# Kernel tuning notes

Hardware: AMD Instinct MI355X
Metric: run time of the kernel (lower is better)

The kernel has to match this reference:

```python
import jax, jax.numpy as jnp
import numpy as np

N_NODES = 100000
N_EDGES = 500000
DIM = 128
HID = 128

def setup_inputs() -> dict:
    key = jax.random.key(0)
    k1, k2, k3, k4, k5, k6 = jax.random.split(key, 6)
    z = jax.random.normal(k1, (N_NODES, DIM), dtype=jnp.float32)
    edge_index = jax.random.randint(k2, (2, N_EDGES), 0, N_NODES, dtype=jnp.int64)
    # Linear params (torch default init: U(-1/sqrt(fan_in), 1/sqrt(fan_in)))
    b1_lim = 1.0 / np.sqrt(3 * DIM)
    b2_lim = 1.0 / np.sqrt(HID)
    W1 = jax.random.uniform(k3, (3 * DIM, HID), jnp.float32, -b1_lim, b1_lim)
    b1 = jax.random.uniform(k4, (HID,), jnp.float32, -b1_lim, b1_lim)
    W2 = jax.random.uniform(k5, (HID, 1), jnp.float32, -b2_lim, b2_lim)
    b2 = jax.random.uniform(k6, (1,), jnp.float32, -b2_lim, b2_lim)
    return {"z": z, "edge_index": edge_index, "W1": W1, "b1": b1, "W2": W2, "b2": b2}

def reference(z, edge_index, W1, b1, W2, b2):
    u, v = edge_index[0], edge_index[1]
    zu = z[u]                      # [E, dim]
    zv = z[v]                      # [E, dim]
    feat = jnp.concatenate([zu, zv, jnp.abs(zu - zv)], axis=1)  # [E, 3*dim]
    h = jax.nn.relu(feat @ W1 + b1)   # [E, hid]
    logit = h @ W2 + b2               # [E, 1]
    return logit.squeeze(-1)          # [E]
```

## Files before the change

### kernel.cpp

```cpp
#include <hip/hip_runtime.h>
#include <hip/hip_bf16.h>
#include <cstdint>


typedef __bf16 bf16_t;
typedef __bf16 bf16x8 __attribute__((ext_vector_type(8)));
typedef float  floatx4 __attribute__((ext_vector_type(4)));

#define DIM 128
#define E_TILE 128
#define N_KSTEP 12
#define N_NTILE 8
#define GRID_B 256

__global__ void cast_z_kernel(const float* __restrict__ z, bf16_t* __restrict__ zb, int n) {
    int idx = (blockIdx.x * 256 + threadIdx.x) * 8;
    if (idx + 8 > n) return;
    const float4* src = reinterpret_cast<const float4*>(z + idx);
    float4 a = src[0], b = src[1];
    bf16x8 o;
    o[0] = (bf16_t)a.x; o[1] = (bf16_t)a.y; o[2] = (bf16_t)a.z; o[3] = (bf16_t)a.w;
    o[4] = (bf16_t)b.x; o[5] = (bf16_t)b.y; o[6] = (bf16_t)b.z; o[7] = (bf16_t)b.w;
    *reinterpret_cast<bf16x8*>(zb + idx) = o;
}

__global__ void pack_w1_kernel(const float* __restrict__ W1, bf16_t* __restrict__ Wp) {
    int f = blockIdx.x * 256 + threadIdx.x;
    if (f >= N_KSTEP * N_NTILE * 64) return;
    int lane = f & 63;
    int nt   = (f >> 6) & 7;
    int ks   = f >> 9;
    int n  = nt * 16 + (lane & 15);
    int k0 = ks * 32 + (lane >> 4) * 8;
    bf16x8 o;
#pragma unroll
    for (int j = 0; j < 8; ++j) o[j] = (bf16_t)W1[(k0 + j) * DIM + n];
    reinterpret_cast<bf16x8*>(Wp)[f] = o;
}

template <bool PRECAST>
__global__ __launch_bounds__(512, 2)
void decode_kernel(const void* __restrict__ zsrc,
                   const int* __restrict__ ei,
                   const bf16_t* __restrict__ Wp,
                   const float* __restrict__ b1,
                   const float* __restrict__ W2,
                   const float* __restrict__ b2,
                   float* __restrict__ out, int E) {
    __shared__ __align__(16) bf16_t Bsm[N_KSTEP * N_NTILE * 64 * 8];
    __shared__ float red[2][2][E_TILE];

    const int tid = threadIdx.x;

    {
        const uint4* src = reinterpret_cast<const uint4*>(Wp);
        uint4* dst = reinterpret_cast<uint4*>(Bsm);
#pragma unroll
        for (int i = 0; i < 12; ++i)
            dst[i * 512 + tid] = src[i * 512 + tid];
    }
    __syncthreads();

    const int wave = tid >> 6, lane = tid & 63;
    const int wm = wave >> 1, wn = wave & 1;
    const int l15 = lane & 15, quad = lane >> 4;
    const float bias2 = b2[0];

    float b1v[4], w2v[4];
#pragma unroll
    for (int nt = 0; nt < 4; ++nt) {
        int n = (wn * 4 + nt) * 16 + l15;
        b1v[nt] = b1[n];
        w2v[nt] = W2[n];
    }

    const int ntiles = (E + E_TILE - 1) / E_TILE;

    auto gatherChunk = [&](bf16x8& du, bf16x8& dv, int nu, int nv, int c) {
        if (PRECAST) {
            const bf16_t* zb = (const bf16_t*)zsrc;
            du = *reinterpret_cast<const bf16x8*>(zb + (size_t)nu * DIM + c * 32 + quad * 8);
            dv = *reinterpret_cast<const bf16x8*>(zb + (size_t)nv * DIM + c * 32 + quad * 8);
        } else {
            const float* zf = (const float*)zsrc;
            const float4* pu = reinterpret_cast<const float4*>(zf + (size_t)nu * DIM + c * 32 + quad * 8);
            const float4* pv = reinterpret_cast<const float4*>(zf + (size_t)nv * DIM + c * 32 + quad * 8);
            float4 a = pu[0], b = pu[1];
            bf16x8 o;
            o[0] = (bf16_t)a.x; o[1] = (bf16_t)a.y; o[2] = (bf16_t)a.z; o[3] = (bf16_t)a.w;
            o[4] = (bf16_t)b.x; o[5] = (bf16_t)b.y; o[6] = (bf16_t)b.z; o[7] = (bf16_t)b.w;
            du = o;
            a = pv[0]; b = pv[1];
            o[0] = (bf16_t)a.x; o[1] = (bf16_t)a.y; o[2] = (bf16_t)a.z; o[3] = (bf16_t)a.w;
            o[4] = (bf16_t)b.x; o[5] = (bf16_t)b.y; o[6] = (bf16_t)b.z; o[7] = (bf16_t)b.w;
            dv = o;
        }
    };

    auto loadB4 = [&](bf16x8* dst, int ks) {
#pragma unroll
        for (int nt = 0; nt < 4; ++nt)
            dst[nt] = *reinterpret_cast<const bf16x8*>(
                &Bsm[(size_t)((ks * N_NTILE + wn * 4 + nt) * 64 + lane) * 8]);
    };

    auto loadIdx = [&](int t, int mt, int& nu, int& nv) {
        int e = t * E_TILE + wm * 32 + mt * 16 + l15;
        if (e >= E) e = E - 1;
        nu = ei[e];
        nv = ei[E + e];
    };

    struct AChunk { bf16x8 u[2], v[2]; };
    AChunk A0, A1;
    int cnu[2], cnv[2], nnu[2], nnv[2];

#pragma unroll
    for (int mt = 0; mt < 2; ++mt) loadIdx(blockIdx.x, mt, cnu[mt], cnv[mt]);
#pragma unroll
    for (int mt = 0; mt < 2; ++mt)
        gatherChunk(A0.u[mt], A0.v[mt], cnu[mt], cnv[mt], 0);

    int p = 0;

    for (int t = blockIdx.x; t < ntiles; t += GRID_B) {
#pragma unroll
        for (int mt = 0; mt < 2; ++mt) loadIdx(t + GRID_B, mt, nnu[mt], nnv[mt]);

        floatx4 acc[2][4];
#pragma unroll
        for (int mt = 0; mt < 2; ++mt)
#pragma unroll
            for (int nt = 0; nt < 4; ++nt) acc[mt][nt] = (floatx4)0.0f;

#pragma unroll
        for (int g = 0; g < 4; ++g) {
            AChunk& cur = (g & 1) ? A1 : A0;
            AChunk& nxt = (g & 1) ? A0 : A1;

            if (g < 3) {
#pragma unroll
                for (int mt = 0; mt < 2; ++mt)
                    gatherChunk(nxt.u[mt], nxt.v[mt], cnu[mt], cnv[mt], g + 1);
            } else {
#pragma unroll
                for (int mt = 0; mt < 2; ++mt)
                    gatherChunk(nxt.u[mt], nxt.v[mt], nnu[mt], nnv[mt], 0);
            }

            {
                bf16x8 bc[4];
                loadB4(bc, g);
#pragma unroll
                for (int mt = 0; mt < 2; ++mt)
#pragma unroll
                    for (int nt = 0; nt < 4; ++nt)
                        acc[mt][nt] = __builtin_amdgcn_mfma_f32_16x16x32_bf16(
                            cur.u[mt], bc[nt], acc[mt][nt], 0, 0, 0);
            }
            {
                bf16x8 bc[4];
                loadB4(bc, 4 + g);
#pragma unroll
                for (int mt = 0; mt < 2; ++mt)
#pragma unroll
                    for (int nt = 0; nt < 4; ++nt)
                        acc[mt][nt] = __builtin_amdgcn_mfma_f32_16x16x32_bf16(
                            cur.v[mt], bc[nt], acc[mt][nt], 0, 0, 0);
            }
            {
                bf16x8 bc[4];
                loadB4(bc, 8 + g);
#pragma unroll
                for (int mt = 0; mt < 2; ++mt) {
                    bf16x8 u = cur.u[mt], v = cur.v[mt];
                    bf16x8 d;
#pragma unroll
                    for (int j = 0; j < 8; ++j)
                        d[j] = (bf16_t)fabsf((float)u[j] - (float)v[j]);
#pragma unroll
                    for (int nt = 0; nt < 4; ++nt)
                        acc[mt][nt] = __builtin_amdgcn_mfma_f32_16x16x32_bf16(
                            d, bc[nt], acc[mt][nt], 0, 0, 0);
                }
            }
        }
#pragma unroll
        for (int mt = 0; mt < 2; ++mt) { cnu[mt] = nnu[mt]; cnv[mt] = nnv[mt]; }

#pragma unroll
        for (int mt = 0; mt < 2; ++mt)
#pragma unroll
            for (int r = 0; r < 4; ++r) {
                float s = 0.f;
#pragma unroll
                for (int nt = 0; nt < 4; ++nt) {
                    float hh = acc[mt][nt][r] + b1v[nt];
                    hh = fmaxf(hh, 0.f);
                    s += hh * w2v[nt];
                }
                s += __shfl_xor(s, 1);
                s += __shfl_xor(s, 2);
                s += __shfl_xor(s, 4);
                s += __shfl_xor(s, 8);
                if (l15 == 0)
                    red[p][wn][wm * 32 + mt * 16 + quad * 4 + r] = s;
            }
        __syncthreads();

        if (tid < E_TILE) {
            int e = t * E_TILE + tid;
            if (e < E) out[e] = red[p][0][tid] + red[p][1][tid] + bias2;
        }
        p ^= 1;
    }
}

extern "C" void kernel_launch(void* const* d_in, const int* in_sizes, int n_in,
                              void* d_out, int out_size, void* d_ws, size_t ws_size,
                              hipStream_t stream) {
    const float* z  = (const float*)d_in[0];
    const int*   ei = (const int*)d_in[1];
    const float* W1 = (const float*)d_in[2];
    const float* b1 = (const float*)d_in[3];
    const float* W2 = (const float*)d_in[4];
    const float* b2 = (const float*)d_in[5];
    float* out = (float*)d_out;

    const int E  = in_sizes[1] / 2;
    const int zn = in_sizes[0];

    const size_t zb_bytes = (size_t)zn * sizeof(bf16_t);
    const size_t wp_bytes = (size_t)N_KSTEP * N_NTILE * 64 * 16;
    const bool precast = ws_size >= zb_bytes + wp_bytes;

    bf16_t* zb = (bf16_t*)d_ws;
    bf16_t* wp = precast ? (bf16_t*)((char*)d_ws + zb_bytes) : (bf16_t*)d_ws;

    hipLaunchKernelGGL(pack_w1_kernel, dim3((N_KSTEP * N_NTILE * 64 + 255) / 256),
                       dim3(256), 0, stream, W1, wp);

    if (precast) {
        hipLaunchKernelGGL(cast_z_kernel, dim3((zn / 8 + 255) / 256), dim3(256),
                           0, stream, z, zb, zn);
        hipLaunchKernelGGL((decode_kernel<true>), dim3(GRID_B), dim3(512), 0,
                           stream, (const void*)zb, ei, wp, b1, W2, b2, out, E);
    } else {
        hipLaunchKernelGGL((decode_kernel<false>), dim3(GRID_B), dim3(512), 0,
                           stream, (const void*)z, ei, wp, b1, W2, b2, out, E);
    }
}
```

Measured before the change: 194.1 us.

## Split hidden dimension across grid halves and combine outputs with atomics

The decode kernel now splits the 128 hidden units across two grid rows (blockIdx.y). Each block stages only its half of packed W1 into shared memory and handles 256-edge tiles with 8 waves, each covering 32 edges. Partial logits are added into the output with atomicAdd after a separate kernel fills the output with b2, which removes the shared-memory reduction and per-tile __syncthreads. In exchange every edge's z rows are gathered twice, once per half, and there is an extra init launch plus atomic traffic.

```diff
diff --git a/kernel.cpp b/kernel.cpp
--- a/kernel.cpp
+++ b/kernel.cpp
@@ -8,10 +8,15 @@
 typedef float  floatx4 __attribute__((ext_vector_type(4)));
 
 #define DIM 128
-#define E_TILE 128
+#define E_TILE 256
 #define N_KSTEP 12
 #define N_NTILE 8
-#define GRID_B 256
+#define GRID_PER_HALF 384
+
+__global__ void init_out_kernel(float* __restrict__ out, const float* __restrict__ b2, int E) {
+    int i = blockIdx.x * 256 + threadIdx.x;
+    if (i < E) out[i] = b2[0];
+}
 
 __global__ void cast_z_kernel(const float* __restrict__ z, bf16_t* __restrict__ zb, int n) {
     int idx = (blockIdx.x * 256 + threadIdx.x) * 8;
@@ -45,31 +50,32 @@
                    const bf16_t* __restrict__ Wp,
                    const float* __restrict__ b1,
                    const float* __restrict__ W2,
-                   const float* __restrict__ b2,
                    float* __restrict__ out, int E) {
-    __shared__ __align__(16) bf16_t Bsm[N_KSTEP * N_NTILE * 64 * 8];
-    __shared__ float red[2][2][E_TILE];
+    __shared__ __align__(16) bf16_t Bsm[N_KSTEP * 4 * 64 * 8];
 
     const int tid = threadIdx.x;
+    const int h   = blockIdx.y;
 
     {
         const uint4* src = reinterpret_cast<const uint4*>(Wp);
         uint4* dst = reinterpret_cast<uint4*>(Bsm);
 #pragma unroll
-        for (int i = 0; i < 12; ++i)
-            dst[i * 512 + tid] = src[i * 512 + tid];
+        for (int i = 0; i < 6; ++i) {
+            int linear = i * 512 + tid;
+            int ks  = linear >> 8;
+            int rem = linear & 255;
+            dst[linear] = src[ks * 512 + h * 256 + rem];
+        }
     }
     __syncthreads();
 
     const int wave = tid >> 6, lane = tid & 63;
-    const int wm = wave >> 1, wn = wave & 1;
     const int l15 = lane & 15, quad = lane >> 4;
-    const float bias2 = b2[0];
 
     float b1v[4], w2v[4];
 #pragma unroll
     for (int nt = 0; nt < 4; ++nt) {
-        int n = (wn * 4 + nt) * 16 + l15;
+        int n = (h * 4 + nt) * 16 + l15;
         b1v[nt] = b1[n];
         w2v[nt] = W2[n];
     }
@@ -101,11 +107,11 @@
 #pragma unroll
         for (int nt = 0; nt < 4; ++nt)
             dst[nt] = *reinterpret_cast<const bf16x8*>(
-                &Bsm[(size_t)((ks * N_NTILE + wn * 4 + nt) * 64 + lane) * 8]);
+                &Bsm[(size_t)((ks * 4 + nt) * 64 + lane) * 8]);
     };
 
     auto loadIdx = [&](int t, int mt, int& nu, int& nv) {
-        int e = t * E_TILE + wm * 32 + mt * 16 + l15;
+        int e = t * E_TILE + wave * 32 + mt * 16 + l15;
         if (e >= E) e = E - 1;
         nu = ei[e];
         nv = ei[E + e];
@@ -121,11 +127,9 @@
     for (int mt = 0; mt < 2; ++mt)
         gatherChunk(A0.u[mt], A0.v[mt], cnu[mt], cnv[mt], 0);
 
-    int p = 0;
-
-    for (int t = blockIdx.x; t < ntiles; t += GRID_B) {
-#pragma unroll
-        for (int mt = 0; mt < 2; ++mt) loadIdx(t + GRID_B, mt, nnu[mt], nnv[mt]);
+    for (int t = blockIdx.x; t < ntiles; t += GRID_PER_HALF) {
+#pragma unroll
+        for (int mt = 0; mt < 2; ++mt) loadIdx(t + GRID_PER_HALF, mt, nnu[mt], nnv[mt]);
 
         floatx4 acc[2][4];
 #pragma unroll
@@ -203,16 +207,11 @@
                 s += __shfl_xor(s, 2);
                 s += __shfl_xor(s, 4);
                 s += __shfl_xor(s, 8);
-                if (l15 == 0)
-                    red[p][wn][wm * 32 + mt * 16 + quad * 4 + r] = s;
-            }
-        __syncthreads();
-
-        if (tid < E_TILE) {
-            int e = t * E_TILE + tid;
-            if (e < E) out[e] = red[p][0][tid] + red[p][1][tid] + bias2;
-        }
-        p ^= 1;
+                if (l15 == 0) {
+                    int e = t * E_TILE + wave * 32 + mt * 16 + quad * 4 + r;
+                    if (e < E) atomicAdd(&out[e], s);
+                }
+            }
     }
 }
 
@@ -237,16 +236,18 @@
     bf16_t* zb = (bf16_t*)d_ws;
     bf16_t* wp = precast ? (bf16_t*)((char*)d_ws + zb_bytes) : (bf16_t*)d_ws;
 
+    hipLaunchKernelGGL(init_out_kernel, dim3((E + 255) / 256), dim3(256),
+                       0, stream, out, b2, E);
     hipLaunchKernelGGL(pack_w1_kernel, dim3((N_KSTEP * N_NTILE * 64 + 255) / 256),
                        dim3(256), 0, stream, W1, wp);
 
     if (precast) {
         hipLaunchKernelGGL(cast_z_kernel, dim3((zn / 8 + 255) / 256), dim3(256),
                            0, stream, z, zb, zn);
-        hipLaunchKernelGGL((decode_kernel<true>), dim3(GRID_B), dim3(512), 0,
-                           stream, (const void*)zb, ei, wp, b1, W2, b2, out, E);
+        hipLaunchKernelGGL((decode_kernel<true>), dim3(GRID_PER_HALF, 2), dim3(512), 0,
+                           stream, (const void*)zb, ei, wp, b1, W2, out, E);
     } else {
-        hipLaunchKernelGGL((decode_kernel<false>), dim3(GRID_B), dim3(512), 0,
-                           stream, (const void*)z, ei, wp, b1, W2, b2, out, E);
-    }
-}
+        hipLaunchKernelGGL((decode_kernel<false>), dim3(GRID_PER_HALF, 2), dim3(512), 0,
+                           stream, (const void*)z, ei, wp, b1, W2, out, E);
+    }
+}
```

Result: slower. 227.2 us (+17.1%).
